# Optimization experiments

Hardware: AMD Instinct MI355X
Metric: run time of the kernel (lower is better)

Reference implementation:

```python
import jax, jax.numpy as jnp
import numpy as np


def setup_inputs() -> dict:
    key = jax.random.key(0)
    B, T, C = 8, 4096, 768
    k1, k2, k3, k4 = jax.random.split(key, 4)
    # Per-channel time-decay (w) and time-first (u) weights; real RWKV uses
    # negative decay but the log-domain max-subtraction math is stable either way.
    w = jax.random.normal(k1, (C,), dtype=jnp.float32)
    u = jax.random.normal(k2, (C,), dtype=jnp.float32)
    k = jax.random.normal(k3, (B, T, C), dtype=jnp.float32)
    v = jax.random.normal(k4, (B, T, C), dtype=jnp.float32)
    return {"B": B, "T": T, "C": C, "w": w, "u": u, "k": k, "v": v}


def reference(B, T, C, w, u, k, v):
    # Faithful JAX port of wkv_pytorch: numerically-stable log-domain RWKV
    # WKV recurrence, vectorized over (B, C) and scanned over T.
    NEG_INF = -1e38
    wf = w.astype(jnp.float32)
    uf = u.astype(jnp.float32)
    kf = k.astype(jnp.float32)
    vf = v.astype(jnp.float32)

    def step(carry, inp):
        aa, bb, pp = carry           # each (B, C)
        kt, vt = inp                 # each (B, C)
        ww = uf + kt                 # u broadcast over batch
        p = jnp.maximum(pp, ww)
        e1 = jnp.exp(pp - p)
        e2 = jnp.exp(ww - p)
        yt = (e1 * aa + e2 * vt) / (e1 * bb + e2)
        ww2 = wf + pp
        p2 = jnp.maximum(ww2, kt)
        e1b = jnp.exp(ww2 - p2)
        e2b = jnp.exp(kt - p2)
        return (e1b * aa + e2b * vt, e1b * bb + e2b, p2), yt

    Bn, Cn = kf.shape[0], kf.shape[2]
    init = (
        jnp.zeros((Bn, Cn), jnp.float32),
        jnp.zeros((Bn, Cn), jnp.float32),
        jnp.full((Bn, Cn), NEG_INF, jnp.float32),
    )
    kT = jnp.swapaxes(kf, 0, 1)  # (T, B, C) for scan over time
    vT = jnp.swapaxes(vf, 0, 1)
    _, y = jax.lax.scan(step, init, (kT, vT))
    y = jnp.swapaxes(y, 0, 1)    # back to (B, T, C)
    return y.astype(k.dtype)
```

## Files before the change

### kernel.cpp

```cpp
#include <hip/hip_runtime.h>
#include <math.h>


#define NEG_INF (-1e38f)
#define NCC 256
#define SCW 16
#define NSC (NCC / SCW)
#define LL  16

typedef float f4 __attribute__((ext_vector_type(4)));

__device__ __forceinline__ void wkv_step(float& aa, float& bb, float& pp,
                                         float wc, float kt, float vt) {
    float ww = wc + pp;
    float p  = fmaxf(ww, kt);
    float d  = ww - kt;
    float e  = __expf(-fabsf(d));
    float e1 = (d >= 0.f) ? 1.f : e;
    float e2 = (d >= 0.f) ? e   : 1.f;
    aa = e1 * aa + e2 * vt;
    bb = e1 * bb + e2;
    pp = p;
}

__device__ __forceinline__ float wkv_ostep(float aa, float bb, float pp,
                                           float uc, float kt, float vt) {
    float ww = uc + kt;
    float d  = pp - ww;
    float e  = __expf(-fabsf(d));
    float e1 = (d >= 0.f) ? 1.f : e;
    float e2 = (d >= 0.f) ? e   : 1.f;
    return __fdividef(e1 * aa + e2 * vt, e1 * bb + e2);
}

__device__ __forceinline__ void wkv_combine(float& aa, float& bb, float& pp,
                                            float dw, float la, float lb, float lp) {
    float ppd = pp + dw;
    float p   = fmaxf(ppd, lp);
    float e1  = __expf(ppd - p);
    float e2  = __expf(lp - p);
    aa = e1 * aa + e2 * la;
    bb = e1 * bb + e2 * lb;
    pp = p;
}

__global__ __launch_bounds__(192)
void wkv_pass1(const float* __restrict__ w,
               const float* __restrict__ kg,
               const float* __restrict__ vg,
               float* __restrict__ sa, float* __restrict__ sb,
               float* __restrict__ sp,
               int B, int T, int C) {
    const int b   = blockIdx.x / NCC;
    const int j   = blockIdx.x % NCC;
    const int tid = threadIdx.x;
    const int C4  = C >> 2;

    const f4* kp = (const f4*)(kg + ((size_t)b * T + (size_t)j * LL) * C) + tid;
    const f4* vp = (const f4*)(vg + ((size_t)b * T + (size_t)j * LL) * C) + tid;
    const f4  wc = ((const f4*)w)[tid];

    f4 kb[LL], vb[LL];
    #pragma unroll
    for (int t = 0; t < LL; ++t) { kb[t] = kp[t * C4]; vb[t] = vp[t * C4]; }
    __builtin_amdgcn_sched_group_barrier(0x20, 2 * LL + 1, 0);

    float aa[4] = {0.f, 0.f, 0.f, 0.f};
    float bb[4] = {0.f, 0.f, 0.f, 0.f};
    float pp[4] = {NEG_INF, NEG_INF, NEG_INF, NEG_INF};
    #pragma unroll
    for (int t = 0; t < LL; ++t) {
        #pragma unroll
        for (int q = 0; q < 4; ++q) {
            float kt = kb[t][q], vt = vb[t][q];
            wkv_step(aa[q], bb[q], pp[q], wc[q], kt, vt);
        }
    }

    const int base = j * (B * C) + b * C;
    f4 oa = {aa[0], aa[1], aa[2], aa[3]};
    f4 ob = {bb[0], bb[1], bb[2], bb[3]};
    f4 op = {pp[0], pp[1], pp[2], pp[3]};
    ((f4*)(sa + base))[tid] = oa;
    ((f4*)(sb + base))[tid] = ob;
    ((f4*)(sp + base))[tid] = op;
}

__global__ void wkv_scan_local(const float* __restrict__ w,
                               float* __restrict__ sa, float* __restrict__ sb,
                               float* __restrict__ sp,
                               int B, int C) {
    const int BC = B * C;
    int tid = blockIdx.x * blockDim.x + threadIdx.x;
    if (tid >= BC * NSC) return;
    const int bc = tid % BC;
    const int sc = tid / BC;
    const float wL = w[bc % C] * (float)LL;

    float la[SCW], lb[SCW], lp[SCW];
    #pragma unroll
    for (int i = 0; i < SCW; ++i) {
        const int idx = (sc * SCW + i) * BC + bc;
        la[i] = sa[idx]; lb[i] = sb[idx]; lp[i] = sp[idx];
    }
    float aa = 0.f, bb = 0.f, pp = NEG_INF;
    #pragma unroll
    for (int i = 0; i < SCW; ++i) {
        wkv_combine(aa, bb, pp, wL, la[i], lb[i], lp[i]);
        const int idx = (sc * SCW + i) * BC + bc;
        sa[idx] = aa; sb[idx] = bb; sp[idx] = pp;
    }
}

__global__ void wkv_scan_super(const float* __restrict__ w,
                               float* __restrict__ sa, float* __restrict__ sb,
                               float* __restrict__ sp,
                               int B, int C) {
    const int BC = B * C;
    int bc = blockIdx.x * blockDim.x + threadIdx.x;
    if (bc >= BC) return;
    const float wSL = w[bc % C] * (float)(LL * SCW);

    float ta[NSC], tb[NSC], tp[NSC];
    #pragma unroll
    for (int sc = 0; sc < NSC; ++sc) {
        const int idx = (sc * SCW + (SCW - 1)) * BC + bc;
        ta[sc] = sa[idx]; tb[sc] = sb[idx]; tp[sc] = sp[idx];
    }
    float aa = 0.f, bb = 0.f, pp = NEG_INF;
    #pragma unroll
    for (int sc = 0; sc < NSC; ++sc) {
        const int idx = (sc * SCW + (SCW - 1)) * BC + bc;
        sa[idx] = aa; sb[idx] = bb; sp[idx] = pp;
        wkv_combine(aa, bb, pp, wSL, ta[sc], tb[sc], tp[sc]);
    }
}

__global__ __launch_bounds__(192)
void wkv_pass3(const float* __restrict__ w, const float* __restrict__ u,
               const float* __restrict__ kg, const float* __restrict__ vg,
               const float* __restrict__ sa, const float* __restrict__ sb,
               const float* __restrict__ sp,
               float* __restrict__ y,
               int B, int T, int C) {
    const int b   = blockIdx.x / NCC;
    const int j   = blockIdx.x % NCC;
    const int tid = threadIdx.x;
    const int C4  = C >> 2;
    const int BC  = B * C;

    const size_t rowbase = ((size_t)b * T + (size_t)j * LL) * C;
    const f4* kp = (const f4*)(kg + rowbase) + tid;
    const f4* vp = (const f4*)(vg + rowbase) + tid;
    f4*       yp = (f4*)(y + rowbase) + tid;
    const f4  wc = ((const f4*)w)[tid];
    const f4  uc = ((const f4*)u)[tid];

    f4 kb[LL], vb[LL];
    #pragma unroll
    for (int t = 0; t < LL; ++t) { kb[t] = kp[t * C4]; vb[t] = vp[t * C4]; }
    __builtin_amdgcn_sched_group_barrier(0x20, 2 * LL, 0);

    const int sc = j / SCW;
    const int i  = j % SCW;
    const int slot_last = (sc * SCW + (SCW - 1)) * BC + b * C;
    f4 Ea = ((const f4*)(sa + slot_last))[tid];
    f4 Eb = ((const f4*)(sb + slot_last))[tid];
    f4 Ep = ((const f4*)(sp + slot_last))[tid];

    float aa[4], bb[4], pp[4];
    if (i == 0) {
        #pragma unroll
        for (int q = 0; q < 4; ++q) { aa[q] = Ea[q]; bb[q] = Eb[q]; pp[q] = Ep[q]; }
    } else {
        const int prev = (j - 1) * BC + b * C;
        f4 la = ((const f4*)(sa + prev))[tid];
        f4 lb = ((const f4*)(sb + prev))[tid];
        f4 lp = ((const f4*)(sp + prev))[tid];
        const float steps = (float)(i * LL);
        #pragma unroll
        for (int q = 0; q < 4; ++q) {
            float a = Ea[q], bq = Eb[q], p = Ep[q];
            wkv_combine(a, bq, p, wc[q] * steps, la[q], lb[q], lp[q]);
            aa[q] = a; bb[q] = bq; pp[q] = p;
        }
    }

    #pragma unroll
    for (int t = 0; t < LL; ++t) {
        f4 yo;
        #pragma unroll
        for (int q = 0; q < 4; ++q) {
            float kt = kb[t][q], vt = vb[t][q];
            yo[q] = wkv_ostep(aa[q], bb[q], pp[q], uc[q], kt, vt);
            wkv_step(aa[q], bb[q], pp[q], wc[q], kt, vt);
        }
        __builtin_nontemporal_store(yo, yp + t * C4);
    }
}

extern "C" void kernel_launch(void* const* d_in, const int* in_sizes, int n_in,
                              void* d_out, int out_size, void* d_ws, size_t ws_size,
                              hipStream_t stream) {
    const float* w = (const float*)d_in[3];
    const float* u = (const float*)d_in[4];
    const float* k = (const float*)d_in[5];
    const float* v = (const float*)d_in[6];
    float* y = (float*)d_out;

    const int C  = in_sizes[3];
    const int BT = in_sizes[5] / C;
    const int T  = 4096;
    const int B  = BT / T;

    const int BC = B * C;
    const size_t total = (size_t)BC * NCC;
    float* sa = (float*)d_ws;
    float* sb = sa + total;
    float* sp = sb + total;

    wkv_pass1<<<B * NCC, C / 4, 0, stream>>>(w, k, v, sa, sb, sp, B, T, C);

    const int n2 = BC * NSC;
    wkv_scan_local<<<(n2 + 255) / 256, 256, 0, stream>>>(w, sa, sb, sp, B, C);
    wkv_scan_super<<<(BC + 255) / 256, 256, 0, stream>>>(w, sa, sb, sp, B, C);

    wkv_pass3<<<B * NCC, C / 4, 0, stream>>>(w, u, k, v, sa, sb, sp, y, B, T, C);
}
```

Measured before the change: 104.2 us.

## Pipeline pass1 chunk loads through double-buffered LDS with direct global-to-LDS loads

Pass1 now has each block process 8 chunks in sequence instead of one. The k/v rows are streamed with global_load_lds into a double-buffered LDS staging area, so the load for the next half-chunk is issued while the current one is being computed. This aims to hide memory latency and cut the number of launched blocks, at the cost of 96 KB of LDS per block and therefore low occupancy. A sched_group_barrier hint in pass3 is also removed, and pass1 hardcodes C=768.

Result: slower. 108.7 us (+4.3%).

```diff
diff --git a/kernel.cpp b/kernel.cpp
--- a/kernel.cpp
+++ b/kernel.cpp
@@ -7,6 +7,8 @@
 #define SCW 16
 #define NSC (NCC / SCW)
 #define LL  16
+#define CH  768
+#define HALFF 6144
 
 typedef float f4 __attribute__((ext_vector_type(4)));
 
@@ -44,6 +46,12 @@
     pp = p;
 }
 
+__device__ __forceinline__ void gld16(const float* g, float* l) {
+    __builtin_amdgcn_global_load_lds(
+        (const __attribute__((address_space(1))) unsigned int*)g,
+        (__attribute__((address_space(3))) unsigned int*)l, 16, 0, 0);
+}
+
 __global__ __launch_bounds__(192)
 void wkv_pass1(const float* __restrict__ w,
                const float* __restrict__ kg,
@@ -51,39 +59,79 @@
                float* __restrict__ sa, float* __restrict__ sb,
                float* __restrict__ sp,
                int B, int T, int C) {
-    const int b   = blockIdx.x / NCC;
-    const int j   = blockIdx.x % NCC;
+    __shared__ float ldsk[2 * HALFF];
+    __shared__ float ldsv[2 * HALFF];
     const int tid = threadIdx.x;
-    const int C4  = C >> 2;
-
-    const f4* kp = (const f4*)(kg + ((size_t)b * T + (size_t)j * LL) * C) + tid;
-    const f4* vp = (const f4*)(vg + ((size_t)b * T + (size_t)j * LL) * C) + tid;
-    const f4  wc = ((const f4*)w)[tid];
-
-    f4 kb[LL], vb[LL];
-    #pragma unroll
-    for (int t = 0; t < LL; ++t) { kb[t] = kp[t * C4]; vb[t] = vp[t * C4]; }
-    __builtin_amdgcn_sched_group_barrier(0x20, 2 * LL + 1, 0);
-
-    float aa[4] = {0.f, 0.f, 0.f, 0.f};
-    float bb[4] = {0.f, 0.f, 0.f, 0.f};
-    float pp[4] = {NEG_INF, NEG_INF, NEG_INF, NEG_INF};
-    #pragma unroll
-    for (int t = 0; t < LL; ++t) {
-        #pragma unroll
-        for (int q = 0; q < 4; ++q) {
-            float kt = kb[t][q], vt = vb[t][q];
-            wkv_step(aa[q], bb[q], pp[q], wc[q], kt, vt);
-        }
-    }
-
-    const int base = j * (B * C) + b * C;
-    f4 oa = {aa[0], aa[1], aa[2], aa[3]};
-    f4 ob = {bb[0], bb[1], bb[2], bb[3]};
-    f4 op = {pp[0], pp[1], pp[2], pp[3]};
-    ((f4*)(sa + base))[tid] = oa;
-    ((f4*)(sb + base))[tid] = ob;
-    ((f4*)(sp + base))[tid] = op;
+    const int wv  = tid >> 6;
+    const int l   = tid & 63;
+    const int g0  = blockIdx.x * 8;
+    const int BC  = B * C;
+
+    f4 wc = *(const f4*)(w + 4 * tid);
+    asm volatile("" :: "v"(wc));
+
+    auto issue = [&](int H) {
+        const int g  = g0 + (H >> 1);
+        const int bb = g >> 8;
+        const int jj = g & 255;
+        const int ro = (H & 1) * 8;
+        const float* gk = kg + ((size_t)bb * T + (size_t)jj * LL + ro) * CH;
+        const float* gv = vg + ((size_t)bb * T + (size_t)jj * LL + ro) * CH;
+        float* lk = ldsk + (H & 1) * HALFF;
+        float* lv = ldsv + (H & 1) * HALFF;
+        #pragma unroll
+        for (int i = 0; i < 8; ++i) {
+            const int idx = 8 * wv + i;
+            gld16(gk + 256 * idx + 4 * l, lk + 256 * idx);
+            gld16(gv + 256 * idx + 4 * l, lv + 256 * idx);
+        }
+    };
+
+    issue(0);
+
+    float aa[4], bq[4], pp[4];
+    for (int h = 0; h < 16; ++h) {
+        if (h < 15) {
+            issue(h + 1);
+            asm volatile("s_waitcnt vmcnt(16)" ::: "memory");
+        } else {
+            asm volatile("s_waitcnt vmcnt(0)" ::: "memory");
+        }
+        __builtin_amdgcn_sched_barrier(0);
+        __builtin_amdgcn_s_barrier();
+        __builtin_amdgcn_sched_barrier(0);
+
+        if ((h & 1) == 0) {
+            #pragma unroll
+            for (int q = 0; q < 4; ++q) { aa[q] = 0.f; bq[q] = 0.f; pp[q] = NEG_INF; }
+        }
+        const float* lk = ldsk + (h & 1) * HALFF;
+        const float* lv = ldsv + (h & 1) * HALFF;
+        #pragma unroll
+        for (int tt = 0; tt < 8; ++tt) {
+            f4 kk = *(const f4*)(lk + tt * CH + 4 * tid);
+            f4 vv = *(const f4*)(lv + tt * CH + 4 * tid);
+            #pragma unroll
+            for (int q = 0; q < 4; ++q) {
+                float kt = kk[q], vt = vv[q];
+                wkv_step(aa[q], bq[q], pp[q], wc[q], kt, vt);
+            }
+        }
+        if (h & 1) {
+            const int g  = g0 + (h >> 1);
+            const int bb = g >> 8;
+            const int jj = g & 255;
+            const int base = jj * BC + bb * C + 4 * tid;
+            f4 oa = {aa[0], aa[1], aa[2], aa[3]};
+            f4 ob = {bq[0], bq[1], bq[2], bq[3]};
+            f4 op = {pp[0], pp[1], pp[2], pp[3]};
+            *(f4*)(sa + base) = oa;
+            *(f4*)(sb + base) = ob;
+            *(f4*)(sp + base) = op;
+        }
+        __builtin_amdgcn_sched_barrier(0);
+        __builtin_amdgcn_s_barrier();
+    }
 }
 
 __global__ void wkv_scan_local(const float* __restrict__ w,
@@ -159,7 +207,6 @@
     f4 kb[LL], vb[LL];
     #pragma unroll
     for (int t = 0; t < LL; ++t) { kb[t] = kp[t * C4]; vb[t] = vp[t * C4]; }
-    __builtin_amdgcn_sched_group_barrier(0x20, 2 * LL, 0);
 
     const int sc = j / SCW;
     const int i  = j % SCW;
@@ -219,7 +266,7 @@
     float* sb = sa + total;
     float* sp = sb + total;
 
-    wkv_pass1<<<B * NCC, C / 4, 0, stream>>>(w, k, v, sa, sb, sp, B, T, C);
+    wkv_pass1<<<(B * NCC) / 8, C / 4, 0, stream>>>(w, k, v, sa, sb, sp, B, T, C);
 
     const int n2 = BC * NSC;
     wkv_scan_local<<<(n2 + 255) / 256, 256, 0, stream>>>(w, sa, sb, sp, B, C);
```
